# Performance work log

Measured on AMD Instinct MI355X. Metric: run time of the kernel, lower is better.

## Reference

```python
import jax, jax.numpy as jnp
import numpy as np

B, T, HOP = 4, 200, 120
N = T * HOP
M1, A1 = 40, 5            # mcep_order+1, apdc_order+1
HID, COND = 256, 192
SR = 24000.0
ALPHA = 0.466             # frequency-warping for 24 kHz
PD = 4                    # Pade order
PADE = jnp.asarray([1.0, 0.4999273, 0.1067005, 0.00956526, 0.0003041358], jnp.float32)
SIGN = jnp.asarray([1.0, -1.0, 1.0, -1.0], jnp.float32)  # + for odd Pade tap index
F0_MEAN, F0_STD = 5.0, 0.25
MCEP_MEAN, MCEP_STD = 0.0, 1.0
APDC_MEAN, APDC_STD = 0.0, 1.0
NOISE_RATIO, SP_RATE, F0_RATE = 0.5, 1.0, 1.0


def mc2b(mc, a):
    """SPTK mc2b: mel-cepstrum -> MLSA filter coefficients (scan over order)."""
    mc_rev = jnp.moveaxis(mc, -1, 0)[::-1]  # [M1, B, T]
    def step(carry, c):
        b = c - a * carry
        return b, b
    _, bs = jax.lax.scan(step, jnp.zeros_like(mc_rev[0]), mc_rev)
    return jnp.moveaxis(bs[::-1], 0, -1)


def _mlsafir(x, b, d):
    # SPTK mlsafir, vectorized over the PD Pade taps.
    # x: [PD], b: [M1], d: [PD, M1+1]
    aa = 1.0 - ALPHA * ALPHA
    d1 = aa * x + ALPHA * d[:, 1]
    def step(prev, di):  # d_new[i] = d[i] + a*(d[i+1] - d_new[i-1]) : order recurrence
        d_i, d_ip1 = di
        new = d_i + ALPHA * (d_ip1 - prev)
        return new, new
    xs = (d[:, 2:M1].T, d[:, 3:M1 + 1].T)  # [M1-2, PD]
    _, dupd = jax.lax.scan(step, d1, xs)    # [M1-2, PD]
    y = jnp.einsum('mp,m->p', dupd, b[2:])
    # delay-line shift: new d = [x, d1, d1, dupd[2..M]]
    new_d = jnp.concatenate([x[:, None], d1[:, None], d1[:, None], dupd.T], axis=1)
    return y, new_d


def _mlsa_step(state, inp):
    d1a, d1b, d2, pt2 = state
    x, b = inp
    x = x * jnp.exp(b[0])           # gain
    # ---- stage 1 (uses b[1] only), SPTK mlsadf1 ----
    aa = 1.0 - ALPHA * ALPHA
    na = aa * d1b[:PD] + ALPHA * d1a[1:]
    npt = na * b[1]
    v1 = npt * PADE[1:]
    x1 = x + jnp.sum(v1 * SIGN)
    y1 = jnp.sum(v1) + x1
    d1a = jnp.concatenate([d1a[:1], na])
    d1b = jnp.concatenate([x1[None], npt])
    # ---- stage 2 (orders >= 2), SPTK mlsadf2 ----
    fy, d2 = _mlsafir(pt2[:PD], b, d2)
    v2 = fy * PADE[1:]
    x2 = y1 + jnp.sum(v2 * SIGN)
    y2 = jnp.sum(v2) + x2
    pt2 = jnp.concatenate([x2[None], fy])
    return (d1a, d1b, d2, pt2), y2


def mlsa_filter(exc, b_up):
    # exc: [N], b_up: [N, M1] -> filtered waveform [N]
    init = (jnp.zeros(PD + 1, jnp.float32), jnp.zeros(PD + 1, jnp.float32),
            jnp.zeros((PD, M1 + 1), jnp.float32), jnp.zeros(PD + 1, jnp.float32))
    _, y = jax.lax.scan(_mlsa_step, init, (exc, b_up))
    return y


def _forward(mceps, apdcs, frame_f0s, noise,
             Wm, bm, Wa, ba, Wf, bf, Wpa, bpa, Wpp, bpp,
             Wrp, brp, Wra, bra, Wap):
    # linear feature embed + sum
    hs = mceps @ Wm + bm + apdcs @ Wa + ba + frame_f0s @ Wf + bf   # [B,T,HID]
    ca = hs @ Wpa + bpa                                             # prenet_a cond [B,T,COND]
    cp = hs @ Wpp + bpp                                             # prenet_p cond
    # denorm (+ exp for log-f0)
    f0 = jnp.exp(frame_f0s[..., 0] * F0_STD + F0_MEAN) * F0_RATE    # [B,T]
    sp = mceps * MCEP_STD + MCEP_MEAN
    ap = apdcs * APDC_STD + APDC_MEAN
    # per-path mel-cepstra with prenet residuals
    mc_p = sp * SP_RATE + 0.1 * jnp.tanh(cp @ Wrp + brp)
    mc_a = sp * SP_RATE + 0.1 * jnp.tanh(ca @ Wra + bra) + ap @ Wap
    b_p = mc2b(mc_p, ALPHA)
    b_a = mc2b(mc_a, ALPHA)
    # excitation at sample rate
    f0_up = jnp.repeat(f0, HOP, axis=1)                             # [B,N]
    phase = jnp.cumsum(f0_up / SR, axis=1)
    w = jnp.floor(phase)
    wprev = jnp.concatenate([jnp.zeros_like(w[:, :1]), w[:, :-1]], axis=1)
    amp = jnp.sqrt(SR / jnp.maximum(f0_up, 1.0))
    pulse = jnp.where(w > wprev, amp, 0.0)
    exc_p = pulse * (1.0 - NOISE_RATIO)
    exc_a = noise * NOISE_RATIO
    # run both (periodic/aperiodic) MLSA synthesis filters in one batched scan
    excs = jnp.concatenate([exc_p, exc_a], axis=0)                  # [2B,N]
    bs = jnp.repeat(jnp.concatenate([b_p, b_a], axis=0), HOP, axis=1)  # [2B,N,M1]
    wavs = jax.vmap(mlsa_filter)(excs, bs)                          # [2B,N]
    return wavs[:B] + wavs[B:]


_forward_jit = jax.jit(_forward)


def setup_inputs() -> dict:
    key = jax.random.key(0)
    ks = jax.random.split(key, 20)
    decay = 0.3 / (1.0 + jnp.arange(M1, dtype=jnp.float32))  # realistic cepstral decay (filter stability)
    return {
        'mceps': jax.random.normal(ks[0], (B, T, M1), jnp.float32) * decay,
        'apdcs': jax.random.normal(ks[1], (B, T, A1), jnp.float32) * 0.3,
        'frame_f0s': jax.random.normal(ks[2], (B, T, 1), jnp.float32),
        'noise': jax.random.normal(ks[3], (B, N), jnp.float32),
        'Wm': jax.random.normal(ks[4], (M1, HID), jnp.float32) / np.sqrt(M1),
        'bm': jnp.zeros((HID,), jnp.float32),
        'Wa': jax.random.normal(ks[5], (A1, HID), jnp.float32) / np.sqrt(A1),
        'ba': jnp.zeros((HID,), jnp.float32),
        'Wf': jax.random.normal(ks[6], (1, HID), jnp.float32),
        'bf': jnp.zeros((HID,), jnp.float32),
        'Wpa': jax.random.normal(ks[7], (HID, COND), jnp.float32) / np.sqrt(HID),
        'bpa': jnp.zeros((COND,), jnp.float32),
        'Wpp': jax.random.normal(ks[8], (HID, COND), jnp.float32) / np.sqrt(HID),
        'bpp': jnp.zeros((COND,), jnp.float32),
        'Wrp': jax.random.normal(ks[9], (COND, M1), jnp.float32) / np.sqrt(COND),
        'brp': jnp.zeros((M1,), jnp.float32),
        'Wra': jax.random.normal(ks[10], (COND, M1), jnp.float32) / np.sqrt(COND),
        'bra': jnp.zeros((M1,), jnp.float32),
        'Wap': jax.random.normal(ks[11], (A1, M1), jnp.float32) * 0.05,
    }


def reference(mceps, apdcs, frame_f0s, noise,
              Wm, bm, Wa, ba, Wf, bf, Wpa, bpa, Wpp, bpp,
              Wrp, brp, Wra, bra, Wap):
    return _forward_jit(mceps, apdcs, frame_f0s, noise,
                        Wm, bm, Wa, ba, Wf, bf, Wpa, bpa, Wpp, bpp,
                        Wrp, brp, Wra, bra, Wap)
```

## Files before the change

### kernel.cpp

```cpp
#include <hip/hip_runtime.h>
#include <math.h>

#define ALPHA 0.466f
#define T_FRAMES 200
#define HOPW 120
#define NSAMP 24000
#define M1 40
#define HID 256
#define CONDW 192

#define NCHUNK 100
#define CHUNKF 2
#define WARMF 4
#define SERF (WARMF + CHUNKF)

#define F8 8
#define BPF ((NSAMP + 255) / 256)

__global__ __launch_bounds__(256) void embed_kernel(
    const float* __restrict__ mceps, const float* __restrict__ apdcs,
    const float* __restrict__ f0s,
    const float* __restrict__ Wm, const float* __restrict__ bm,
    const float* __restrict__ Wa, const float* __restrict__ ba,
    const float* __restrict__ Wf, const float* __restrict__ bf,
    const float* __restrict__ Wpa, const float* __restrict__ bpa,
    const float* __restrict__ Wpp, const float* __restrict__ bpp,
    const float* __restrict__ Wrp, const float* __restrict__ brp,
    const float* __restrict__ Wra, const float* __restrict__ bra,
    const float* __restrict__ Wap, float* __restrict__ bcoef)
{
    __shared__ float s_mc[F8][M1];
    __shared__ float s_ap[F8][5];
    __shared__ float s_f0[F8];
    __shared__ float s_h[F8][HID];
    __shared__ float s_ca[F8][CONDW];
    __shared__ float s_cp[F8][CONDW];
    __shared__ float s_mcp[F8][M1];
    __shared__ float s_mca[F8][M1];

    const int tid = threadIdx.x;
    const int R0 = blockIdx.x * F8;

    for (int j = tid; j < F8 * M1; j += 256) s_mc[j / M1][j % M1] = mceps[R0 * M1 + j];
    if (tid < F8 * 5) s_ap[tid / 5][tid % 5] = apdcs[R0 * 5 + tid];
    if (tid < F8)     s_f0[tid] = f0s[R0 + tid];
    __syncthreads();

    {
        float acc[F8];
        const float bias = bm[tid] + ba[tid] + bf[tid];
        #pragma unroll
        for (int r = 0; r < F8; ++r) acc[r] = bias;
        for (int k = 0; k < M1; ++k) {
            float w = Wm[k * HID + tid];
            #pragma unroll
            for (int r = 0; r < F8; ++r) acc[r] = fmaf(s_mc[r][k], w, acc[r]);
        }
        #pragma unroll
        for (int k = 0; k < 5; ++k) {
            float w = Wa[k * HID + tid];
            #pragma unroll
            for (int r = 0; r < F8; ++r) acc[r] = fmaf(s_ap[r][k], w, acc[r]);
        }
        float wf = Wf[tid];
        #pragma unroll
        for (int r = 0; r < F8; ++r) s_h[r][tid] = fmaf(s_f0[r], wf, acc[r]);
    }
    __syncthreads();

    if (tid < CONDW) {
        float aA[F8], aP[F8];
        #pragma unroll
        for (int r = 0; r < F8; ++r) { aA[r] = bpa[tid]; aP[r] = bpp[tid]; }
        for (int k = 0; k < HID; k += 4) {
            float4 h4[F8];
            #pragma unroll
            for (int r = 0; r < F8; ++r) h4[r] = *(const float4*)&s_h[r][k];
            #pragma unroll
            for (int kk = 0; kk < 4; ++kk) {
                float wa = Wpa[(k + kk) * CONDW + tid];
                float wp = Wpp[(k + kk) * CONDW + tid];
                #pragma unroll
                for (int r = 0; r < F8; ++r) {
                    float hv = (&h4[r].x)[kk];
                    aA[r] = fmaf(hv, wa, aA[r]);
                    aP[r] = fmaf(hv, wp, aP[r]);
                }
            }
        }
        #pragma unroll
        for (int r = 0; r < F8; ++r) { s_ca[r][tid] = aA[r]; s_cp[r][tid] = aP[r]; }
    }
    __syncthreads();

    if (tid < M1) {
        const int u = tid;
        float acc[F8];
        #pragma unroll
        for (int r = 0; r < F8; ++r) acc[r] = brp[u];
        for (int k = 0; k < CONDW; k += 4) {
            float4 c4[F8];
            #pragma unroll
            for (int r = 0; r < F8; ++r) c4[r] = *(const float4*)&s_cp[r][k];
            #pragma unroll
            for (int kk = 0; kk < 4; ++kk) {
                float w = Wrp[(k + kk) * M1 + u];
                #pragma unroll
                for (int r = 0; r < F8; ++r) acc[r] = fmaf((&c4[r].x)[kk], w, acc[r]);
            }
        }
        #pragma unroll
        for (int r = 0; r < F8; ++r)
            s_mcp[r][u] = s_mc[r][u] + 0.1f * tanhf(acc[r]);
    } else if (tid >= 64 && tid < 64 + M1) {
        const int u = tid - 64;
        float acc[F8];
        #pragma unroll
        for (int r = 0; r < F8; ++r) acc[r] = bra[u];
        for (int k = 0; k < CONDW; k += 4) {
            float4 c4[F8];
            #pragma unroll
            for (int r = 0; r < F8; ++r) c4[r] = *(const float4*)&s_ca[r][k];
            #pragma unroll
            for (int kk = 0; kk < 4; ++kk) {
                float w = Wra[(k + kk) * M1 + u];
                #pragma unroll
                for (int r = 0; r < F8; ++r) acc[r] = fmaf((&c4[r].x)[kk], w, acc[r]);
            }
        }
        #pragma unroll
        for (int r = 0; r < F8; ++r) {
            float aw = 0.f;
            #pragma unroll
            for (int j = 0; j < 5; ++j) aw = fmaf(s_ap[r][j], Wap[j * M1 + u], aw);
            s_mca[r][u] = s_mc[r][u] + 0.1f * tanhf(acc[r]) + aw;
        }
    }
    __syncthreads();

    if (tid < 16) {
        const int r = tid >> 1, path = tid & 1;
        const int R = R0 + r;
        const int batch = R / T_FRAMES, t = R - batch * T_FRAMES;
        const float* src = path ? s_mca[r] : s_mcp[r];
        float* dst = bcoef + ((path * 4 + batch) * T_FRAMES + t) * M1;
        float prev = src[M1 - 1];
        dst[M1 - 1] = prev;
        for (int m = M1 - 2; m >= 0; --m) {
            prev = src[m] - ALPHA * prev;
            dst[m] = prev;
        }
    }
}

__global__ __launch_bounds__(256) void exc_kernel(
    const float* __restrict__ f0s, const float* __restrict__ noise,
    float* __restrict__ exc)
{
    const int ff = blockIdx.x / BPF;
    const int n = (blockIdx.x % BPF) * 256 + threadIdx.x;
    const int tid = threadIdx.x;

    if (ff >= 4) {
        if (n < NSAMP) exc[ff * NSAMP + n] = 0.5f * noise[(ff - 4) * NSAMP + n];
        return;
    }

    __shared__ double s_base[T_FRAMES];
    __shared__ double s_step[T_FRAMES];
    __shared__ float  s_amp[T_FRAMES];

    if (tid < 64) {
        const int L = tid;
        double st[4], loc[4];
        float am[4];
        double s = 0.0;
        #pragma unroll
        for (int j = 0; j < 4; ++j) {
            int ft = L * 4 + j;
            if (ft < T_FRAMES) {
                double fv = exp((double)f0s[ff * T_FRAMES + ft] * 0.25 + 5.0);
                st[j] = fv / 24000.0;
                am[j] = (float)(0.5 * sqrt(24000.0 / fmax(fv, 1.0)));
            } else { st[j] = 0.0; am[j] = 0.f; }
            loc[j] = s;
            s += st[j];
        }
        double tot = s;
        #pragma unroll
        for (int off = 1; off < 64; off <<= 1) {
            double v = __shfl_up(s, off, 64);
            if (L >= off) s += v;
        }
        double excl = s - tot;
        #pragma unroll
        for (int j = 0; j < 4; ++j) {
            int ft = L * 4 + j;
            if (ft < T_FRAMES) {
                s_base[ft] = 120.0 * (excl + loc[j]);
                s_step[ft] = st[j];
                s_amp[ft]  = am[j];
            }
        }
    }
    __syncthreads();

    if (n < NSAMP) {
        int ft = n / HOPW, k = n - ft * HOPW;
        double st = s_step[ft], bs = s_base[ft];
        double ph  = bs + (double)(k + 1) * st;
        double php = bs + (double)k * st;
        exc[ff * NSAMP + n] = (floor(ph) > floor(php)) ? s_amp[ft] : 0.0f;
    }
}

template <int CTRL>
__device__ __forceinline__ float rshr(float x) {
    return __int_as_float(
        __builtin_amdgcn_mov_dpp(__float_as_int(x), CTRL, 0xF, 0xF, true));
}
__device__ __forceinline__ float rlane(float x, int l) {
    return __int_as_float(__builtin_amdgcn_readlane(__float_as_int(x), l));
}

template <bool OUT>
__device__ __forceinline__ void run_frame(
    const float* __restrict__ sx, float AB,
    float BP1, float BP2, float BP3, float BP4,
    float Ba, float Bb, float Bc, float K, float IPw, int i16, int row,
    float& E0, float& E1, float& E2, float& dlp, float& xin,
    float& m1, float& m2, float& m3, float& m4, float& w0,
    float* __restrict__ yout)
{
    const float A = ALPHA;
    const float AA = 1.0f - A * A;
    const float A2 = A * A;
    const float R1 = -(A * A * A);
    const float R2 = R1 * R1;
    const float R4 = R2 * R2;
    const float R8 = R4 * R4;

    float xc = sx[0];
    #pragma unroll 8
    for (int k = 0; k < HOPW; ++k) {
        float xn = sx[k + 1];
        float x = xc;

        float na0 = AA * w0 + A * m1;
        float na1 = AB * m1 + A * m2;
        float na2 = AB * m2 + A * m3;
        float na3 = AB * m3 + A * m4;
        float v10 = na0 * BP1, v11 = na1 * BP2, v12 = na2 * BP3, v13 = na3 * BP4;
        float x1 = x + ((v10 - v11) + (v12 - v13));
        float y1 = ((v10 + v11) + (v12 + v13)) + x1;
        m1 = na0; m2 = na1; m3 = na2; m4 = na3; w0 = x1;

        float pE2 = rshr<0x111>(E2);
        float ca = fmaf(A, E0, (i16 == 0) ? dlp : pE2);
        float cb = fmaf(A, E1, E0);
        float cc = fmaf(A, E2, E1);
        float ua = ca;
        float ub = fmaf(-A, ua, cb);
        float uc = fmaf(-A, ub, cc);
        float X = uc;
        X = fmaf(R1, rshr<0x111>(X), X);
        X = fmaf(R2, rshr<0x112>(X), X);
        X = fmaf(R4, rshr<0x114>(X), X);
        X = fmaf(R8, rshr<0x118>(X), X);
        float dl = fmaf(AA, xin, A * dlp);
        float Xt = fmaf(K, dl, X);
        float Si = rshr<0x111>(Xt);
        Si = (i16 == 0) ? dl : Si;
        float ta = fmaf(-A, Si, ua);
        float tb = fmaf(A2, Si, ub);

        float fp = ta * Ba;
        fp = fmaf(tb, Bb, fp);
        fp = fmaf(Xt, Bc, fp);
        float S = fp;
        S += rshr<0x111>(S);
        S += rshr<0x112>(S);
        S += rshr<0x114>(S);
        S += rshr<0x118>(S);

        float xprev = rshr<0x142>(S) * IPw;

        float v20 = rlane(S, 15);
        float v21 = rlane(S, 31);
        float v22 = rlane(S, 47);
        float v23 = rlane(S, 63);
        float e = v20 + v22, o = v21 + v23;
        float x2 = y1 + (e - o);
        if (OUT) {
            float y2 = (e + o) + x2;
            yout[k] = y2;
        }

        xin = (row == 0) ? x2 : xprev;
        E0 = ta; E1 = tb; E2 = Xt;
        dlp = dl;
        xc = xn;
    }
}

__global__ __launch_bounds__(64) void mlsa_kernel(
    const float* __restrict__ bcoef, const float* __restrict__ exc,
    float* __restrict__ y2g)
{
    __shared__ float sexc[HOPW + 2];

    const int tid = threadIdx.x;
    const int i16 = tid & 15;
    const int row = tid >> 4;
    const int chunk = blockIdx.x >> 3;
    const int f = blockIdx.x & 7;

    const float P1 = 0.4999273f, P2 = 0.1067005f, P3 = 0.00956526f, P4 = 0.0003041358f;
    const float Pw  = (row == 0) ? P1 : (row == 1) ? P2 : (row == 2) ? P3 : P4;
    const float IPw = (row == 1) ? (1.f / P1) : (row == 2) ? (1.f / P2) : (1.f / P3);

    const float R1 = -(ALPHA * ALPHA * ALPHA);
    float K = R1;
    for (int j = 0; j < i16; ++j) K *= R1;

    float E0 = 0.f, E1 = 0.f, E2 = 0.f;
    float dlp = 0.f, xin = 0.f;
    float m1 = 0.f, m2 = 0.f, m3 = 0.f, m4 = 0.f, w0 = 0.f;

    const int outF0 = chunk * CHUNKF;

    #pragma unroll 1
    for (int i = 0; i < SERF; ++i) {
        const int ftA = outF0 - WARMF + i;

        const int ftc = (ftA < 0) ? 0 : ftA;
        const float* bp = bcoef + (f * T_FRAMES + ftc) * M1;
        const float b1 = bp[1];
        const float G  = expf(bp[0]);
        const float AA = 1.0f - ALPHA * ALPHA;
        const float AB = AA * b1;
        const float BP1 = b1 * P1, BP2 = b1 * P2, BP3 = b1 * P3, BP4 = b1 * P4;

        for (int j = tid; j < HOPW; j += 64)
            sexc[j] = (ftA >= 0) ? exc[f * NSAMP + ftA * HOPW + j] * G : 0.f;
        if (tid == 0) sexc[HOPW] = 0.f;

        const int ja = 3 * i16 + 2;
        const float Ba = ((i16 <= 12) ? bp[ja]     : 0.f) * Pw;
        const float Bb = ((i16 <= 12) ? bp[ja + 1] : 0.f) * Pw;
        const float Bc = ((i16 <= 11) ? bp[ja + 2] : 0.f) * Pw;
        float* yout = y2g + f * NSAMP + ftA * HOPW;

        if (i >= WARMF)
            run_frame<true>(sexc, AB, BP1, BP2, BP3, BP4, Ba, Bb, Bc, K, IPw,
                            i16, row, E0, E1, E2, dlp, xin, m1, m2, m3, m4, w0, yout);
        else
            run_frame<false>(sexc, AB, BP1, BP2, BP3, BP4, Ba, Bb, Bc, K, IPw,
                             i16, row, E0, E1, E2, dlp, xin, m1, m2, m3, m4, w0, yout);
    }
}

__global__ __launch_bounds__(256) void combine_kernel(
    const float* __restrict__ y2g, float* __restrict__ out)
{
    int i = blockIdx.x * 256 + threadIdx.x;
    if (i >= 4 * NSAMP) return;
    int b = i / NSAMP, n = i - b * NSAMP;
    out[i] = y2g[b * NSAMP + n] + y2g[(4 + b) * NSAMP + n];
}

extern "C" void kernel_launch(void* const* d_in, const int* in_sizes, int n_in,
                              void* d_out, int out_size, void* d_ws, size_t ws_size,
                              hipStream_t stream) {
    const float* mceps = (const float*)d_in[0];
    const float* apdcs = (const float*)d_in[1];
    const float* f0s   = (const float*)d_in[2];
    const float* noise = (const float*)d_in[3];
    const float* Wm  = (const float*)d_in[4];
    const float* bm  = (const float*)d_in[5];
    const float* Wa  = (const float*)d_in[6];
    const float* ba  = (const float*)d_in[7];
    const float* Wf  = (const float*)d_in[8];
    const float* bf  = (const float*)d_in[9];
    const float* Wpa = (const float*)d_in[10];
    const float* bpa = (const float*)d_in[11];
    const float* Wpp = (const float*)d_in[12];
    const float* bpp = (const float*)d_in[13];
    const float* Wrp = (const float*)d_in[14];
    const float* brp = (const float*)d_in[15];
    const float* Wra = (const float*)d_in[16];
    const float* bra = (const float*)d_in[17];
    const float* Wap = (const float*)d_in[18];
    float* out = (float*)d_out;

    char* ws = (char*)d_ws;
    float* bcoef = (float*)(ws + 0);
    float* exc   = (float*)(ws + 256000);
    float* y2g   = (float*)(ws + 1024000);

    embed_kernel<<<dim3(4 * T_FRAMES / F8), dim3(256), 0, stream>>>(
        mceps, apdcs, f0s, Wm, bm, Wa, ba, Wf, bf,
        Wpa, bpa, Wpp, bpp, Wrp, brp, Wra, bra, Wap, bcoef);

    exc_kernel<<<dim3(8 * BPF), dim3(256), 0, stream>>>(f0s, noise, exc);

    mlsa_kernel<<<dim3(NCHUNK * 8), dim3(64), 0, stream>>>(bcoef, exc, y2g);

    combine_kernel<<<dim3((4 * NSAMP + 255) / 256), dim3(256), 0, stream>>>(
        y2g, out);
}
```

Measured before the change: 221.9 us.

## Fuse embed and excitation kernels and fold combine into MLSA kernel

The embedding and excitation kernels are merged into one prep launch, with block index deciding which work a block does. The MLSA kernel now runs the periodic and aperiodic paths of the same batch as two wavefronts in one 128-thread block. Their outputs are summed through shared memory and written straight to the output, so the separate combine kernel and its intermediate buffer go away. This removes two launches and a global round trip, at the cost of extra block-level barriers per output frame and only lane 0 writing the per-sample results.

```diff
diff --git a/kernel.cpp b/kernel.cpp
--- a/kernel.cpp
+++ b/kernel.cpp
@@ -15,11 +15,12 @@
 #define SERF (WARMF + CHUNKF)
 
 #define F8 8
+#define EMB_BLOCKS (4 * T_FRAMES / F8)
 #define BPF ((NSAMP + 255) / 256)
 
-__global__ __launch_bounds__(256) void embed_kernel(
+__global__ __launch_bounds__(256) void prep_kernel(
     const float* __restrict__ mceps, const float* __restrict__ apdcs,
-    const float* __restrict__ f0s,
+    const float* __restrict__ f0s, const float* __restrict__ noise,
     const float* __restrict__ Wm, const float* __restrict__ bm,
     const float* __restrict__ Wa, const float* __restrict__ ba,
     const float* __restrict__ Wf, const float* __restrict__ bf,
@@ -27,8 +28,70 @@
     const float* __restrict__ Wpp, const float* __restrict__ bpp,
     const float* __restrict__ Wrp, const float* __restrict__ brp,
     const float* __restrict__ Wra, const float* __restrict__ bra,
-    const float* __restrict__ Wap, float* __restrict__ bcoef)
+    const float* __restrict__ Wap,
+    float* __restrict__ bcoef, float* __restrict__ exc)
 {
+    const int tid = threadIdx.x;
+
+    if (blockIdx.x >= EMB_BLOCKS) {
+        const int xb = blockIdx.x - EMB_BLOCKS;
+        const int ff = xb / BPF;
+        const int n = (xb % BPF) * 256 + tid;
+
+        if (ff >= 4) {
+            if (n < NSAMP) exc[ff * NSAMP + n] = 0.5f * noise[(ff - 4) * NSAMP + n];
+            return;
+        }
+
+        __shared__ double s_base[T_FRAMES];
+        __shared__ double s_step[T_FRAMES];
+        __shared__ float  s_amp[T_FRAMES];
+
+        if (tid < 64) {
+            const int L = tid;
+            double st[4], loc[4];
+            float am[4];
+            double s = 0.0;
+            #pragma unroll
+            for (int j = 0; j < 4; ++j) {
+                int ft = L * 4 + j;
+                if (ft < T_FRAMES) {
+                    double fv = exp((double)f0s[ff * T_FRAMES + ft] * 0.25 + 5.0);
+                    st[j] = fv / 24000.0;
+                    am[j] = (float)(0.5 * sqrt(24000.0 / fmax(fv, 1.0)));
+                } else { st[j] = 0.0; am[j] = 0.f; }
+                loc[j] = s;
+                s += st[j];
+            }
+            double tot = s;
+            #pragma unroll
+            for (int off = 1; off < 64; off <<= 1) {
+                double v = __shfl_up(s, off, 64);
+                if (L >= off) s += v;
+            }
+            double excl = s - tot;
+            #pragma unroll
+            for (int j = 0; j < 4; ++j) {
+                int ft = L * 4 + j;
+                if (ft < T_FRAMES) {
+                    s_base[ft] = 120.0 * (excl + loc[j]);
+                    s_step[ft] = st[j];
+                    s_amp[ft]  = am[j];
+                }
+            }
+        }
+        __syncthreads();
+
+        if (n < NSAMP) {
+            int ft = n / HOPW, k = n - ft * HOPW;
+            double st = s_step[ft], bs = s_base[ft];
+            double ph  = bs + (double)(k + 1) * st;
+            double php = bs + (double)k * st;
+            exc[ff * NSAMP + n] = (floor(ph) > floor(php)) ? s_amp[ft] : 0.0f;
+        }
+        return;
+    }
+
     __shared__ float s_mc[F8][M1];
     __shared__ float s_ap[F8][5];
     __shared__ float s_f0[F8];
@@ -38,7 +101,6 @@
     __shared__ float s_mcp[F8][M1];
     __shared__ float s_mca[F8][M1];
 
-    const int tid = threadIdx.x;
     const int R0 = blockIdx.x * F8;
 
     for (int j = tid; j < F8 * M1; j += 256) s_mc[j / M1][j % M1] = mceps[R0 * M1 + j];
@@ -153,67 +215,6 @@
     }
 }
 
-__global__ __launch_bounds__(256) void exc_kernel(
-    const float* __restrict__ f0s, const float* __restrict__ noise,
-    float* __restrict__ exc)
-{
-    const int ff = blockIdx.x / BPF;
-    const int n = (blockIdx.x % BPF) * 256 + threadIdx.x;
-    const int tid = threadIdx.x;
-
-    if (ff >= 4) {
-        if (n < NSAMP) exc[ff * NSAMP + n] = 0.5f * noise[(ff - 4) * NSAMP + n];
-        return;
-    }
-
-    __shared__ double s_base[T_FRAMES];
-    __shared__ double s_step[T_FRAMES];
-    __shared__ float  s_amp[T_FRAMES];
-
-    if (tid < 64) {
-        const int L = tid;
-        double st[4], loc[4];
-        float am[4];
-        double s = 0.0;
-        #pragma unroll
-        for (int j = 0; j < 4; ++j) {
-            int ft = L * 4 + j;
-            if (ft < T_FRAMES) {
-                double fv = exp((double)f0s[ff * T_FRAMES + ft] * 0.25 + 5.0);
-                st[j] = fv / 24000.0;
-                am[j] = (float)(0.5 * sqrt(24000.0 / fmax(fv, 1.0)));
-            } else { st[j] = 0.0; am[j] = 0.f; }
-            loc[j] = s;
-            s += st[j];
-        }
-        double tot = s;
-        #pragma unroll
-        for (int off = 1; off < 64; off <<= 1) {
-            double v = __shfl_up(s, off, 64);
-            if (L >= off) s += v;
-        }
-        double excl = s - tot;
-        #pragma unroll
-        for (int j = 0; j < 4; ++j) {
-            int ft = L * 4 + j;
-            if (ft < T_FRAMES) {
-                s_base[ft] = 120.0 * (excl + loc[j]);
-                s_step[ft] = st[j];
-                s_amp[ft]  = am[j];
-            }
-        }
-    }
-    __syncthreads();
-
-    if (n < NSAMP) {
-        int ft = n / HOPW, k = n - ft * HOPW;
-        double st = s_step[ft], bs = s_base[ft];
-        double ph  = bs + (double)(k + 1) * st;
-        double php = bs + (double)k * st;
-        exc[ff * NSAMP + n] = (floor(ph) > floor(php)) ? s_amp[ft] : 0.0f;
-    }
-}
-
 template <int CTRL>
 __device__ __forceinline__ float rshr(float x) {
     return __int_as_float(
@@ -228,9 +229,10 @@
     const float* __restrict__ sx, float AB,
     float BP1, float BP2, float BP3, float BP4,
     float Ba, float Bb, float Bc, float K, float IPw, int i16, int row,
+    bool lane0,
     float& E0, float& E1, float& E2, float& dlp, float& xin,
     float& m1, float& m2, float& m3, float& m4, float& w0,
-    float* __restrict__ yout)
+    float* __restrict__ ybw)
 {
     const float A = ALPHA;
     const float AA = 1.0f - A * A;
@@ -293,7 +295,7 @@
         float x2 = y1 + (e - o);
         if (OUT) {
             float y2 = (e + o) + x2;
-            yout[k] = y2;
+            if (lane0) ybw[k] = y2;
         }
 
         xin = (row == 0) ? x2 : xprev;
@@ -303,17 +305,22 @@
     }
 }
 
-__global__ __launch_bounds__(64) void mlsa_kernel(
+__global__ __launch_bounds__(128) void mlsa_kernel(
     const float* __restrict__ bcoef, const float* __restrict__ exc,
-    float* __restrict__ y2g)
+    float* __restrict__ out)
 {
-    __shared__ float sexc[HOPW + 2];
+    __shared__ float sexc[2][HOPW + 2];
+    __shared__ float ybuf[2][HOPW];
 
     const int tid = threadIdx.x;
-    const int i16 = tid & 15;
-    const int row = tid >> 4;
-    const int chunk = blockIdx.x >> 3;
-    const int f = blockIdx.x & 7;
+    const int w = tid >> 6;
+    const int t64 = tid & 63;
+    const int i16 = t64 & 15;
+    const int row = t64 >> 4;
+    const int chunk = blockIdx.x >> 2;
+    const int b = blockIdx.x & 3;
+    const int f = b + 4 * w;
+    const bool lane0 = (t64 == 0);
 
     const float P1 = 0.4999273f, P2 = 0.1067005f, P3 = 0.00956526f, P4 = 0.0003041358f;
     const float Pw  = (row == 0) ? P1 : (row == 1) ? P2 : (row == 2) ? P3 : P4;
@@ -341,32 +348,29 @@
         const float AB = AA * b1;
         const float BP1 = b1 * P1, BP2 = b1 * P2, BP3 = b1 * P3, BP4 = b1 * P4;
 
-        for (int j = tid; j < HOPW; j += 64)
-            sexc[j] = (ftA >= 0) ? exc[f * NSAMP + ftA * HOPW + j] * G : 0.f;
-        if (tid == 0) sexc[HOPW] = 0.f;
+        for (int j = t64; j < HOPW; j += 64)
+            sexc[w][j] = (ftA >= 0) ? exc[f * NSAMP + ftA * HOPW + j] * G : 0.f;
+        if (lane0) sexc[w][HOPW] = 0.f;
 
         const int ja = 3 * i16 + 2;
         const float Ba = ((i16 <= 12) ? bp[ja]     : 0.f) * Pw;
         const float Bb = ((i16 <= 12) ? bp[ja + 1] : 0.f) * Pw;
         const float Bc = ((i16 <= 11) ? bp[ja + 2] : 0.f) * Pw;
-        float* yout = y2g + f * NSAMP + ftA * HOPW;
-
-        if (i >= WARMF)
-            run_frame<true>(sexc, AB, BP1, BP2, BP3, BP4, Ba, Bb, Bc, K, IPw,
-                            i16, row, E0, E1, E2, dlp, xin, m1, m2, m3, m4, w0, yout);
-        else
-            run_frame<false>(sexc, AB, BP1, BP2, BP3, BP4, Ba, Bb, Bc, K, IPw,
-                             i16, row, E0, E1, E2, dlp, xin, m1, m2, m3, m4, w0, yout);
-    }
-}
-
-__global__ __launch_bounds__(256) void combine_kernel(
-    const float* __restrict__ y2g, float* __restrict__ out)
-{
-    int i = blockIdx.x * 256 + threadIdx.x;
-    if (i >= 4 * NSAMP) return;
-    int b = i / NSAMP, n = i - b * NSAMP;
-    out[i] = y2g[b * NSAMP + n] + y2g[(4 + b) * NSAMP + n];
+
+        if (i >= WARMF) {
+            run_frame<true>(sexc[w], AB, BP1, BP2, BP3, BP4, Ba, Bb, Bc, K, IPw,
+                            i16, row, lane0, E0, E1, E2, dlp, xin,
+                            m1, m2, m3, m4, w0, ybuf[w]);
+            __syncthreads();
+            if (tid < HOPW)
+                out[b * NSAMP + ftA * HOPW + tid] = ybuf[0][tid] + ybuf[1][tid];
+            __syncthreads();
+        } else {
+            run_frame<false>(sexc[w], AB, BP1, BP2, BP3, BP4, Ba, Bb, Bc, K, IPw,
+                             i16, row, lane0, E0, E1, E2, dlp, xin,
+                             m1, m2, m3, m4, w0, ybuf[w]);
+        }
+    }
 }
 
 extern "C" void kernel_launch(void* const* d_in, const int* in_sizes, int n_in,
@@ -396,16 +400,10 @@
     char* ws = (char*)d_ws;
     float* bcoef = (float*)(ws + 0);
     float* exc   = (float*)(ws + 256000);
-    float* y2g   = (float*)(ws + 1024000);
-
-    embed_kernel<<<dim3(4 * T_FRAMES / F8), dim3(256), 0, stream>>>(
-        mceps, apdcs, f0s, Wm, bm, Wa, ba, Wf, bf,
-        Wpa, bpa, Wpp, bpp, Wrp, brp, Wra, bra, Wap, bcoef);
-
-    exc_kernel<<<dim3(8 * BPF), dim3(256), 0, stream>>>(f0s, noise, exc);
-
-    mlsa_kernel<<<dim3(NCHUNK * 8), dim3(64), 0, stream>>>(bcoef, exc, y2g);
-
-    combine_kernel<<<dim3((4 * NSAMP + 255) / 256), dim3(256), 0, stream>>>(
-        y2g, out);
-}
+
+    prep_kernel<<<dim3(EMB_BLOCKS + 8 * BPF), dim3(256), 0, stream>>>(
+        mceps, apdcs, f0s, noise, Wm, bm, Wa, ba, Wf, bf,
+        Wpa, bpa, Wpp, bpp, Wrp, brp, Wra, bra, Wap, bcoef, exc);
+
+    mlsa_kernel<<<dim3(NCHUNK * 4), dim3(128), 0, stream>>>(bcoef, exc, out);
+}
```

Result: slower. 286.1 us (+28.9%).
